# Optimization experiments

Measured on AMD Instinct MI355X. Metric: run time of the kernel, lower is better.

## Reference

```python
import jax, jax.numpy as jnp
import numpy as np

W_ENTROPY, W_MI, W_COV, W_ORTHO, W_L1, W_L2 = 1.0, 0.2, 0.2, 0.1, 0.1, 0.1


def setup_inputs() -> dict:
    key = jax.random.key(0)
    k1, k2, k3, k4 = jax.random.split(key, 4)
    B, NCLS, C = 16384, 1000, 1280
    logits = jax.random.normal(k1, (B, NCLS), dtype=jnp.float32)
    output = jax.nn.log_softmax(logits, axis=1)  # nll_loss expects log-probs
    target = jax.random.randint(k2, (B,), 0, NCLS, dtype=jnp.int64)
    weights = jax.random.normal(k3, (NCLS, C), dtype=jnp.float32) * 0.02
    features = jax.random.normal(k4, (B, C), dtype=jnp.float32)
    return {"output": output, "target": target, "weights": weights, "features": features}


def _kl_loss(features):
    # torch: sum_{i,j} F.kl_div(L[:, i], L[:, j], log_target=True, reduction='mean')
    # kl_div(input, tgt, log_target=True) = mean_b exp(tgt)*(tgt - input)
    # => sum_{i,j,b} P[b,j]*(L[b,j]-L[b,i]) / B
    #  = (C * sum(P*L) - sum(L)) / B   (since sum_j P[b,j] == 1)
    B, C = features.shape
    L = jax.nn.log_softmax(features, axis=1)
    P = jnp.exp(L)
    return (C * jnp.sum(P * L) - jnp.sum(L)) / B


def _cov_loss(features):
    B = features.shape[0]
    cf = features - jnp.mean(features, axis=0, keepdims=True)
    cov = (cf.T @ cf) / B  # [C, C]
    eye = jnp.eye(cov.shape[0], dtype=cov.dtype)
    return jnp.sum((cov - eye) ** 2)  # ||.||_F^2


def _ortho_loss(weights):
    w = weights.reshape(weights.shape[0], -1)
    cov = w @ w.T  # row type
    eye = jnp.eye(cov.shape[0], dtype=cov.dtype)
    return jnp.sum((cov - eye) ** 2)


def reference(output, target, weights, features):
    loss_nll = -jnp.mean(jnp.take_along_axis(output, target[:, None], axis=1))
    loss_kl = _kl_loss(features)
    loss_cov = _cov_loss(features)
    loss_ortho = _ortho_loss(weights)
    loss_l1 = jnp.sum(jnp.abs(weights))
    loss_l2 = jnp.sqrt(jnp.sum(weights ** 2))
    loss = (W_ENTROPY * loss_nll + W_MI * loss_kl + W_COV * loss_cov
            + W_ORTHO * loss_ortho + W_L1 * loss_l1 + W_L2 * loss_l2)
    return loss
```

## Files before the change

### kernel.cpp

```cpp
#include <hip/hip_runtime.h>
#include <stdint.h>
#include <stddef.h>

#define B_N    16384
#define NCLS_N 1000
#define C_N    1280

#define ACC_OFF    0ULL
#define TICKET_OFF 64ULL
#define COLSUM_OFF 128ULL
#define FBT_OFF    8192ULL
#define WB_OFF     41951232ULL
#define G_OFF      44572672ULL
#define H_OFF      51126272ULL

enum { A_NLL = 0, A_KL = 1, A_L1 = 2, A_L2SQ = 3, A_SUMSQF = 4, A_FMU2 = 5, A_GFRO = 6, A_HFRO = 7 };

typedef short s16x8 __attribute__((ext_vector_type(8)));
typedef float f32x4 __attribute__((ext_vector_type(4)));

__device__ __forceinline__ unsigned short f2bf(float f) {
    union { float f; unsigned int u; } v; v.f = f;
    unsigned int u = v.u;
    u += 0x7fffu + ((u >> 16) & 1u);
    return (unsigned short)(u >> 16);
}

__device__ __forceinline__ float wave_red(float v) {
#pragma unroll
    for (int o = 32; o; o >>= 1) v += __shfl_down(v, o, 64);
    return v;
}


__device__ __forceinline__ void nll_body(const float* __restrict__ lp,
                                         const int* __restrict__ tgt,
                                         float* __restrict__ acc, int bidx) {
    int b = bidx * 256 + threadIdx.x;
    int t = tgt[b];
    float v = lp[(size_t)b * NCLS_N + t];
    v = wave_red(v);
    __shared__ float sm_nll[4];
    int wid = threadIdx.x >> 6, lane = threadIdx.x & 63;
    if (lane == 0) sm_nll[wid] = v;
    __syncthreads();
    if (threadIdx.x == 0) atomicAdd(&acc[A_NLL], sm_nll[0] + sm_nll[1] + sm_nll[2] + sm_nll[3]);
}

__device__ __forceinline__ void wpass_body(const float* __restrict__ W,
                                           short* __restrict__ Wb,
                                           float* __restrict__ acc, int idx) {
    int bx = idx & 3;
    int kc = idx >> 2;
    int m = bx * 256 + threadIdx.x;
    bool live = (m < NCLS_N);
    const float4* Wr = (const float4*)(W + (size_t)m * C_N);
    float l1 = 0.f, l2 = 0.f;
#pragma unroll
    for (int kj = 0; kj < 4; kj++) {
        s16x8 pk = { 0, 0, 0, 0, 0, 0, 0, 0 };
        if (live) {
            float4 a = Wr[kc * 8 + kj * 2];
            float4 b = Wr[kc * 8 + kj * 2 + 1];
            l1 += fabsf(a.x) + fabsf(a.y) + fabsf(a.z) + fabsf(a.w)
                + fabsf(b.x) + fabsf(b.y) + fabsf(b.z) + fabsf(b.w);
            l2 += a.x * a.x + a.y * a.y + a.z * a.z + a.w * a.w
                + b.x * b.x + b.y * b.y + b.z * b.z + b.w * b.w;
            pk[0] = (short)f2bf(a.x); pk[1] = (short)f2bf(a.y);
            pk[2] = (short)f2bf(a.z); pk[3] = (short)f2bf(a.w);
            pk[4] = (short)f2bf(b.x); pk[5] = (short)f2bf(b.y);
            pk[6] = (short)f2bf(b.z); pk[7] = (short)f2bf(b.w);
        }
        *(s16x8*)(Wb + ((size_t)(kc * 4 + kj) * 1024 + m) * 8) = pk;
    }
    l1 = wave_red(l1);
    l2 = wave_red(l2);
    __shared__ float sm_w[4][2];
    int wid = threadIdx.x >> 6, lane = threadIdx.x & 63;
    if (lane == 0) { sm_w[wid][0] = l1; sm_w[wid][1] = l2; }
    __syncthreads();
    if (threadIdx.x == 0) {
        atomicAdd(&acc[A_L1],   sm_w[0][0] + sm_w[1][0] + sm_w[2][0] + sm_w[3][0]);
        atomicAdd(&acc[A_L2SQ], sm_w[0][1] + sm_w[1][1] + sm_w[2][1] + sm_w[3][1]);
    }
}

__device__ __forceinline__ void fpass_body(const float* __restrict__ F,
                                           short* __restrict__ Fbt,
                                           float* __restrict__ colsum,
                                           float* __restrict__ acc, int idx) {
    int bx = idx % 5;
    int by = idx / 5;
    int c = bx * 256 + threadIdx.x;
    int kc0 = by * 4;
    float cs = 0.f, sq = 0.f;
    for (int ch = 0; ch < 4; ch++) {
        int kc = kc0 + ch;
        int kbase = kc * 32;
#pragma unroll
        for (int kj = 0; kj < 4; kj++) {
            float v[8];
#pragma unroll
            for (int e = 0; e < 8; e++) v[e] = F[(size_t)(kbase + kj * 8 + e) * C_N + c];
            s16x8 pk;
#pragma unroll
            for (int e = 0; e < 8; e++) {
                cs += v[e];
                sq += v[e] * v[e];
                pk[e] = (short)f2bf(v[e]);
            }
            *(s16x8*)(Fbt + ((size_t)(kc * 4 + kj) * C_N + c) * 8) = pk;
        }
    }
    atomicAdd(&colsum[c], cs);
    sq = wave_red(sq);
    __shared__ float sm_f[4];
    int wid = threadIdx.x >> 6, lane = threadIdx.x & 63;
    if (lane == 0) sm_f[wid] = sq;
    __syncthreads();
    if (threadIdx.x == 0) atomicAdd(&acc[A_SUMSQF], sm_f[0] + sm_f[1] + sm_f[2] + sm_f[3]);
}

__device__ __forceinline__ void klpass_body(const float* __restrict__ F,
                                            float* __restrict__ acc, int idx) {
    int wid = threadIdx.x >> 6, lane = threadIdx.x & 63;
    int gwave = idx * 4 + wid;
    float kl_acc = 0.f;
    for (int b = gwave; b < B_N; b += 4096) {
        const float4* Fr = (const float4*)(F + (size_t)b * C_N);
        float s = 0.f, tt = 0.f, sf = 0.f;
#pragma unroll
        for (int i = 0; i < 5; i++) {
            float4 f = Fr[lane + 64 * i];
            float e0 = __expf(f.x), e1 = __expf(f.y), e2 = __expf(f.z), e3 = __expf(f.w);
            s  += e0 + e1 + e2 + e3;
            tt += e0 * f.x + e1 * f.y + e2 * f.z + e3 * f.w;
            sf += f.x + f.y + f.z + f.w;
        }
        s = wave_red(s); tt = wave_red(tt); sf = wave_red(sf);
        if (lane == 0) kl_acc += (float)C_N * (tt / s) - sf;
    }
    __shared__ float sm_kl[4];
    if (lane == 0) sm_kl[wid] = kl_acc;
    __syncthreads();
    if (threadIdx.x == 0)
        atomicAdd(&acc[A_KL], sm_kl[0] + sm_kl[1] + sm_kl[2] + sm_kl[3]);
}

__device__ __forceinline__ void gram_body(const short* __restrict__ X,
                                          float* __restrict__ S,
                                          int Mp, int T, int tile, int kc_blk, int chunkK) {
    __shared__ __align__(16) short A0[128 * 32];
    __shared__ __align__(16) short A1[128 * 32];
    __shared__ __align__(16) short B0[128 * 32];
    __shared__ __align__(16) short B1[128 * 32];
    int tid = threadIdx.x;
    int bi = 0, rem = tile;
    while (rem >= T - bi) { rem -= T - bi; bi++; }
    int bj = bi + rem;
    int i0 = bi * 128, j0 = bj * 128;

    int wave = tid >> 6, lane = tid & 63;
    int wm = wave >> 1, wn = wave & 1;
    int quad = lane >> 4, l16 = lane & 15;

    const size_t kstep = (size_t)Mp * 32;
    const short *pa0, *pa1, *pb0, *pb1;
    int lo0 = tid * 8, lo1 = (256 + tid) * 8;
    {
        int g0 = tid, g1 = 256 + tid;
        int r0 = g0 >> 2, r1 = g1 >> 2;
        int kj0 = (g0 & 3) ^ (r0 & 3), kj1 = (g1 & 3) ^ (r1 & 3);
        size_t base = (size_t)(kc_blk * chunkK >> 5) * kstep;
        pa0 = X + base + ((size_t)kj0 * Mp + i0 + r0) * 8;
        pa1 = X + base + ((size_t)kj1 * Mp + i0 + r1) * 8;
        pb0 = X + base + ((size_t)kj0 * Mp + j0 + r0) * 8;
        pb1 = X + base + ((size_t)kj1 * Mp + j0 + r1) * 8;
    }

    f32x4 acc[4][4];
#pragma unroll
    for (int i = 0; i < 4; i++)
#pragma unroll
        for (int j = 0; j < 4; j++) acc[i][j] = { 0.f, 0.f, 0.f, 0.f };

    auto stage = [&](short* Ad, short* Bd) {
        __builtin_amdgcn_global_load_lds((const __attribute__((address_space(1))) unsigned int*)pa0,
                                         (__attribute__((address_space(3))) unsigned int*)(Ad + lo0), 16, 0, 0);
        __builtin_amdgcn_global_load_lds((const __attribute__((address_space(1))) unsigned int*)pa1,
                                         (__attribute__((address_space(3))) unsigned int*)(Ad + lo1), 16, 0, 0);
        __builtin_amdgcn_global_load_lds((const __attribute__((address_space(1))) unsigned int*)pb0,
                                         (__attribute__((address_space(3))) unsigned int*)(Bd + lo0), 16, 0, 0);
        __builtin_amdgcn_global_load_lds((const __attribute__((address_space(1))) unsigned int*)pb1,
                                         (__attribute__((address_space(3))) unsigned int*)(Bd + lo1), 16, 0, 0);
        pa0 += kstep; pa1 += kstep; pb0 += kstep; pb1 += kstep;
    };

    auto compute = [&](const short* Ab, const short* Bb) {
        s16x8 af[4], bfr[4];
#pragma unroll
        for (int f = 0; f < 4; f++) {
            int mrow = wm * 64 + f * 16 + l16;
            af[f] = *(const s16x8*)(Ab + mrow * 32 + (quad ^ (mrow & 3)) * 8);
            int nrow = wn * 64 + f * 16 + l16;
            bfr[f] = *(const s16x8*)(Bb + nrow * 32 + (quad ^ (nrow & 3)) * 8);
        }
        __builtin_amdgcn_s_setprio(1);
#pragma unroll
        for (int i = 0; i < 4; i++)
#pragma unroll
            for (int j = 0; j < 4; j++)
                acc[i][j] = __builtin_amdgcn_mfma_f32_16x16x32_bf16(af[i], bfr[j], acc[i][j], 0, 0, 0);
        __builtin_amdgcn_s_setprio(0);
    };

    int nt = chunkK >> 5;
    stage(A0, B0);
    __syncthreads();
    for (int t = 0; t < nt; t += 2) {
        stage(A1, B1);
        compute(A0, B0);
        __syncthreads();
        if (t + 2 < nt) stage(A0, B0);
        compute(A1, B1);
        __syncthreads();
    }

#pragma unroll
    for (int i = 0; i < 4; i++)
#pragma unroll
        for (int j = 0; j < 4; j++)
#pragma unroll
            for (int r = 0; r < 4; r++) {
                int grow = i0 + wm * 64 + i * 16 + quad * 4 + r;
                int gcol = j0 + wn * 64 + j * 16 + l16;
                atomicAdd(&S[(size_t)grow * Mp + gcol], acc[i][j][r]);
            }
}

__device__ __forceinline__ void fro_tile(const float* __restrict__ S,
                                         const float* __restrict__ mu_src,
                                         int Mp, int T, int tile,
                                         float* __restrict__ slotF,
                                         float* __restrict__ slotQ) {
    int bi = 0, rem = tile;
    while (rem >= T - bi) { rem -= T - bi; bi++; }
    int bj = bi + rem;
    size_t base = (size_t)bi * 128 * Mp + (size_t)bj * 128;
    const float invB = 1.f / (float)B_N;
    float sum = 0.f, q = 0.f;
    for (int l = threadIdx.x * 4; l < 128 * 128; l += 1024) {
        int row = l >> 7, col = l & 127;
        float4 v = *(const float4*)(S + base + (size_t)row * Mp + col);
        sum += v.x * v.x + v.y * v.y + v.z * v.z + v.w * v.w;
        if (mu_src) {
            float mr = mu_src[bi * 128 + row] * invB;
            float4 mc = *(const float4*)(mu_src + bj * 128 + col);
            q += mr * (v.x * mc.x + v.y * mc.y + v.z * mc.z + v.w * mc.w) * invB;
        }
    }
    sum = wave_red(sum);
    q = wave_red(q);
    __shared__ float sm_fro[4][2];
    int wid = threadIdx.x >> 6, lane = threadIdx.x & 63;
    if (lane == 0) { sm_fro[wid][0] = sum; sm_fro[wid][1] = q; }
    __syncthreads();
    if (threadIdx.x == 0) {
        float w = (bi == bj) ? 1.f : 2.f;
        atomicAdd(slotF, w * (sm_fro[0][0] + sm_fro[1][0] + sm_fro[2][0] + sm_fro[3][0]));
        if (mu_src)
            atomicAdd(slotQ, w * (sm_fro[0][1] + sm_fro[1][1] + sm_fro[2][1] + sm_fro[3][1]));
    }
}


__global__ __launch_bounds__(256) void prep_kernel(const float* __restrict__ lp,
                                                   const int* __restrict__ tgt,
                                                   const float* __restrict__ W,
                                                   const float* __restrict__ F,
                                                   short* __restrict__ Wb,
                                                   short* __restrict__ Fbt,
                                                   float* __restrict__ colsum,
                                                   float* __restrict__ acc,
                                                   float* __restrict__ G,
                                                   float* __restrict__ H) {
    int b = blockIdx.x;
    if (b < 1024) {
        klpass_body(F, acc, b);
    } else if (b < 1664) {
        fpass_body(F, Fbt, colsum, acc, b - 1024);
    } else if (b < 1824) {
        wpass_body(W, Wb, acc, b - 1664);
    } else if (b < 1888) {
        nll_body(lp, tgt, acc, b - 1824);
    } else if (b < 1988) {
        float4* p = (float4*)G + (size_t)(b - 1888) * 4096;
        float4 z = { 0.f, 0.f, 0.f, 0.f };
        for (int i = threadIdx.x; i < 4096; i += 256) p[i] = z;
    } else {
        float4* p = (float4*)H + (size_t)(b - 1988) * 4096;
        float4 z = { 0.f, 0.f, 0.f, 0.f };
        for (int i = threadIdx.x; i < 4096; i += 256) p[i] = z;
    }
}

__global__ __launch_bounds__(256) void main_kernel(const short* __restrict__ Fbt,
                                                   float* __restrict__ G,
                                                   const short* __restrict__ Wb,
                                                   float* __restrict__ H) {
    int b = blockIdx.x;
    if (b < 880) {
        gram_body(Fbt, G, C_N, 10, b >> 4, b & 15, 1024);
    } else {
        int l = b - 880;
        gram_body(Wb, H, 1024, 8, l >> 2, l & 3, 320);
    }
}

__global__ __launch_bounds__(256) void fro_final_kernel(const float* __restrict__ G,
                                                        const float* __restrict__ H,
                                                        float* __restrict__ acc,
                                                        const float* __restrict__ colsum,
                                                        unsigned* __restrict__ ticket,
                                                        float* __restrict__ out) {
    int b = blockIdx.x;
    if (b < 55) fro_tile(G, colsum, C_N, 10, b, acc + A_GFRO, acc + A_FMU2);
    else        fro_tile(H, nullptr, 1024, 8, b - 55, acc + A_HFRO, nullptr);

    __shared__ int amlast;
    if (threadIdx.x == 0) {
        __threadfence();
        unsigned prev = atomicAdd(ticket, 1u);
        amlast = (prev == 90u);
    }
    __syncthreads();
    if (!amlast) return;
    __threadfence();

    float s = 0.f;
    for (int c = threadIdx.x; c < C_N; c += 256) { float v = colsum[c]; s += v * v; }
    s = wave_red(s);
    __shared__ float sm[4];
    int wid = threadIdx.x >> 6, lane = threadIdx.x & 63;
    if (lane == 0) sm[wid] = s;
    __syncthreads();
    if (threadIdx.x == 0) {
        double musq_raw = (double)(sm[0] + sm[1] + sm[2] + sm[3]);
        double Bd = (double)B_N;
        double gfro = (double)atomicAdd(&acc[A_GFRO], 0.0f);
        double hfro = (double)atomicAdd(&acc[A_HFRO], 0.0f);
        double fmu2 = (double)atomicAdd(&acc[A_FMU2], 0.0f);
        double nll = -((double)acc[A_NLL] / Bd);
        double kl  = (double)acc[A_KL] / Bd;
        double trG = (double)acc[A_SUMSQF];
        double musq = musq_raw / (Bd * Bd);
        double cov = gfro / (Bd * Bd)
                   - (2.0 / Bd) * fmu2
                   + musq * musq
                   - 2.0 * (trG / Bd - musq)
                   + (double)C_N;
        double ortho = hfro - 2.0 * (double)acc[A_L2SQ] + (double)NCLS_N;
        double loss = 1.0 * nll + 0.2 * kl + 0.2 * cov + 0.1 * ortho
                    + 0.1 * (double)acc[A_L1] + 0.1 * sqrt((double)acc[A_L2SQ]);
        out[0] = (float)loss;
    }
}

extern "C" void kernel_launch(void* const* d_in, const int* in_sizes, int n_in,
                              void* d_out, int out_size, void* d_ws, size_t ws_size,
                              hipStream_t stream) {
    (void)in_sizes; (void)n_in; (void)out_size; (void)ws_size;
    const float* output_lp = (const float*)d_in[0];
    const int*   target    = (const int*)d_in[1];
    const float* W         = (const float*)d_in[2];
    const float* F         = (const float*)d_in[3];

    char*     ws     = (char*)d_ws;
    float*    acc    = (float*)(ws + ACC_OFF);
    unsigned* ticket = (unsigned*)(ws + TICKET_OFF);
    float*    colsum = (float*)(ws + COLSUM_OFF);
    short*    Fbt    = (short*)(ws + FBT_OFF);
    short*    Wb     = (short*)(ws + WB_OFF);
    float*    G      = (float*)(ws + G_OFF);
    float*    H      = (float*)(ws + H_OFF);

    hipMemsetAsync(ws, 0, 8192, stream);

    prep_kernel<<<2052, 256, 0, stream>>>(output_lp, target, W, F, Wb, Fbt, colsum, acc, G, H);
    main_kernel<<<1024, 256, 0, stream>>>(Fbt, G, Wb, H);
    fro_final_kernel<<<91, 256, 0, stream>>>(G, H, acc, colsum, ticket, (float*)d_out);
}
```

Measured before the change: 294.9 us.

## Write per-split Gram partials instead of atomics; balance K-split; derive sum(F) from colsum

When the workspace is large enough, each split-K Gram block writes its 128x128 partial tile with plain stores to its own slice, and the Frobenius pass sums the slices. This removes the float atomicAdds and the zeroing of G/H, which prep_kernel no longer needs to do since it launches fewer blocks. In the fallback atomic path, K chunks are unequal to balance triangular tiles. The KL term no longer sums features per row and instead takes sum(F) from colsum in the final kernel. The cost is more workspace, extra partial-slice memory traffic in the final reduction, and a different float summation order.

```diff
diff --git a/kernel.cpp b/kernel.cpp
--- a/kernel.cpp
+++ b/kernel.cpp
@@ -13,6 +13,8 @@
 #define WB_OFF     41951232ULL
 #define G_OFF      44572672ULL
 #define H_OFF      51126272ULL
+#define HP_OFF     102244352ULL
+#define WS_PART_NEED 111681536ULL
 
 enum { A_NLL = 0, A_KL = 1, A_L1 = 2, A_L2SQ = 3, A_SUMSQF = 4, A_FMU2 = 5, A_GFRO = 6, A_HFRO = 7 };
 
@@ -128,17 +130,16 @@
     float kl_acc = 0.f;
     for (int b = gwave; b < B_N; b += 4096) {
         const float4* Fr = (const float4*)(F + (size_t)b * C_N);
-        float s = 0.f, tt = 0.f, sf = 0.f;
+        float s = 0.f, tt = 0.f;
 #pragma unroll
         for (int i = 0; i < 5; i++) {
             float4 f = Fr[lane + 64 * i];
             float e0 = __expf(f.x), e1 = __expf(f.y), e2 = __expf(f.z), e3 = __expf(f.w);
             s  += e0 + e1 + e2 + e3;
             tt += e0 * f.x + e1 * f.y + e2 * f.z + e3 * f.w;
-            sf += f.x + f.y + f.z + f.w;
-        }
-        s = wave_red(s); tt = wave_red(tt); sf = wave_red(sf);
-        if (lane == 0) kl_acc += (float)C_N * (tt / s) - sf;
+        }
+        s = wave_red(s); tt = wave_red(tt);
+        if (lane == 0) kl_acc += (float)C_N * (tt / s);
     }
     __shared__ float sm_kl[4];
     if (lane == 0) sm_kl[wid] = kl_acc;
@@ -147,9 +148,11 @@
         atomicAdd(&acc[A_KL], sm_kl[0] + sm_kl[1] + sm_kl[2] + sm_kl[3]);
 }
 
+template<bool PART>
 __device__ __forceinline__ void gram_body(const short* __restrict__ X,
                                           float* __restrict__ S,
-                                          int Mp, int T, int tile, int kc_blk, int chunkK) {
+                                          int Mp, int T, int ntri,
+                                          int tile, int kc_blk, int k0step, int nt) {
     __shared__ __align__(16) short A0[128 * 32];
     __shared__ __align__(16) short A1[128 * 32];
     __shared__ __align__(16) short B0[128 * 32];
@@ -171,7 +174,7 @@
         int g0 = tid, g1 = 256 + tid;
         int r0 = g0 >> 2, r1 = g1 >> 2;
         int kj0 = (g0 & 3) ^ (r0 & 3), kj1 = (g1 & 3) ^ (r1 & 3);
-        size_t base = (size_t)(kc_blk * chunkK >> 5) * kstep;
+        size_t base = (size_t)k0step * kstep;
         pa0 = X + base + ((size_t)kj0 * Mp + i0 + r0) * 8;
         pa1 = X + base + ((size_t)kj1 * Mp + i0 + r1) * 8;
         pb0 = X + base + ((size_t)kj0 * Mp + j0 + r0) * 8;
@@ -214,7 +217,6 @@
         __builtin_amdgcn_s_setprio(0);
     };
 
-    int nt = chunkK >> 5;
     stage(A0, B0);
     __syncthreads();
     for (int t = 0; t < nt; t += 2) {
@@ -226,32 +228,57 @@
         __syncthreads();
     }
 
-#pragma unroll
-    for (int i = 0; i < 4; i++)
-#pragma unroll
-        for (int j = 0; j < 4; j++)
-#pragma unroll
-            for (int r = 0; r < 4; r++) {
-                int grow = i0 + wm * 64 + i * 16 + quad * 4 + r;
-                int gcol = j0 + wn * 64 + j * 16 + l16;
-                atomicAdd(&S[(size_t)grow * Mp + gcol], acc[i][j][r]);
-            }
-}
-
-__device__ __forceinline__ void fro_tile(const float* __restrict__ S,
-                                         const float* __restrict__ mu_src,
-                                         int Mp, int T, int tile,
-                                         float* __restrict__ slotF,
-                                         float* __restrict__ slotQ) {
+    if (PART) {
+        float* Sp = S + (((size_t)kc_blk * ntri + tile) << 14);
+#pragma unroll
+        for (int i = 0; i < 4; i++)
+#pragma unroll
+            for (int j = 0; j < 4; j++)
+#pragma unroll
+                for (int r = 0; r < 4; r++) {
+                    int lrow = wm * 64 + i * 16 + quad * 4 + r;
+                    int lcol = wn * 64 + j * 16 + l16;
+                    Sp[lrow * 128 + lcol] = acc[i][j][r];
+                }
+    } else {
+#pragma unroll
+        for (int i = 0; i < 4; i++)
+#pragma unroll
+            for (int j = 0; j < 4; j++)
+#pragma unroll
+                for (int r = 0; r < 4; r++) {
+                    int grow = i0 + wm * 64 + i * 16 + quad * 4 + r;
+                    int gcol = j0 + wn * 64 + j * 16 + l16;
+                    atomicAdd(&S[(size_t)grow * Mp + gcol], acc[i][j][r]);
+                }
+    }
+}
+
+__device__ __forceinline__ void fro_tile_any(const float* __restrict__ S,
+                                             const float* __restrict__ mu_src,
+                                             int Mp, int T, int ntri, int tile, int nks, bool part,
+                                             float* __restrict__ slotF,
+                                             float* __restrict__ slotQ) {
     int bi = 0, rem = tile;
     while (rem >= T - bi) { rem -= T - bi; bi++; }
     int bj = bi + rem;
-    size_t base = (size_t)bi * 128 * Mp + (size_t)bj * 128;
+    size_t baseA = (size_t)bi * 128 * Mp + (size_t)bj * 128;
+    const float* baseP = S + ((size_t)tile << 14);
+    size_t pstride = (size_t)ntri << 14;
     const float invB = 1.f / (float)B_N;
     float sum = 0.f, q = 0.f;
     for (int l = threadIdx.x * 4; l < 128 * 128; l += 1024) {
         int row = l >> 7, col = l & 127;
-        float4 v = *(const float4*)(S + base + (size_t)row * Mp + col);
+        float4 v;
+        if (part) {
+            v = *(const float4*)(baseP + l);
+            for (int ks = 1; ks < nks; ks++) {
+                float4 u = *(const float4*)(baseP + (size_t)ks * pstride + l);
+                v.x += u.x; v.y += u.y; v.z += u.z; v.w += u.w;
+            }
+        } else {
+            v = *(const float4*)(S + baseA + (size_t)row * Mp + col);
+        }
         sum += v.x * v.x + v.y * v.y + v.z * v.z + v.w * v.w;
         if (mu_src) {
             float mr = mu_src[bi * 128 + row] * invB;
@@ -304,19 +331,31 @@
     }
 }
 
+template<bool PART>
 __global__ __launch_bounds__(256) void main_kernel(const short* __restrict__ Fbt,
                                                    float* __restrict__ G,
                                                    const short* __restrict__ Wb,
                                                    float* __restrict__ H) {
+    const int G_NT[16] = {18,22,26,30,20,24,28,32,46,42,38,34,44,40,36,32};
+    const int G_K0[16] = {0,18,40,66,96,116,140,168,200,246,288,326,360,404,444,480};
+    const int H_NT[4]  = {8,10,12,10};
+    const int H_K0[4]  = {0,8,18,30};
     int b = blockIdx.x;
     if (b < 880) {
-        gram_body(Fbt, G, C_N, 10, b >> 4, b & 15, 1024);
+        int tile = b >> 4, kc = b & 15;
+        int k0 = PART ? kc * 32 : G_K0[kc];
+        int nt = PART ? 32      : G_NT[kc];
+        gram_body<PART>(Fbt, G, C_N, 10, 55, tile, kc, k0, nt);
     } else {
         int l = b - 880;
-        gram_body(Wb, H, 1024, 8, l >> 2, l & 3, 320);
-    }
-}
-
+        int tile = l >> 2, kc = l & 3;
+        int k0 = PART ? kc * 10 : H_K0[kc];
+        int nt = PART ? 10      : H_NT[kc];
+        gram_body<PART>(Wb, H, 1024, 8, 36, tile, kc, k0, nt);
+    }
+}
+
+template<bool PART>
 __global__ __launch_bounds__(256) void fro_final_kernel(const float* __restrict__ G,
                                                         const float* __restrict__ H,
                                                         float* __restrict__ acc,
@@ -324,8 +363,8 @@
                                                         unsigned* __restrict__ ticket,
                                                         float* __restrict__ out) {
     int b = blockIdx.x;
-    if (b < 55) fro_tile(G, colsum, C_N, 10, b, acc + A_GFRO, acc + A_FMU2);
-    else        fro_tile(H, nullptr, 1024, 8, b - 55, acc + A_HFRO, nullptr);
+    if (b < 55) fro_tile_any(G, colsum, C_N, 10, 55, b, 16, PART, acc + A_GFRO, acc + A_FMU2);
+    else        fro_tile_any(H, nullptr, 1024, 8, 36, b - 55, 4, PART, acc + A_HFRO, nullptr);
 
     __shared__ int amlast;
     if (threadIdx.x == 0) {
@@ -337,21 +376,23 @@
     if (!amlast) return;
     __threadfence();
 
-    float s = 0.f;
-    for (int c = threadIdx.x; c < C_N; c += 256) { float v = colsum[c]; s += v * v; }
+    float s = 0.f, s1 = 0.f;
+    for (int c = threadIdx.x; c < C_N; c += 256) { float v = colsum[c]; s += v * v; s1 += v; }
     s = wave_red(s);
-    __shared__ float sm[4];
-    int wid = threadIdx.x >> 6, lane = threadIdx.x & 63;
-    if (lane == 0) sm[wid] = s;
+    s1 = wave_red(s1);
+    __shared__ float sm[4][2];
+    int wid = threadIdx.x >> 6, lane = threadIdx.x & 63;
+    if (lane == 0) { sm[wid][0] = s; sm[wid][1] = s1; }
     __syncthreads();
     if (threadIdx.x == 0) {
-        double musq_raw = (double)(sm[0] + sm[1] + sm[2] + sm[3]);
+        double musq_raw = (double)(sm[0][0] + sm[1][0] + sm[2][0] + sm[3][0]);
+        double sumF     = (double)(sm[0][1] + sm[1][1] + sm[2][1] + sm[3][1]);
         double Bd = (double)B_N;
         double gfro = (double)atomicAdd(&acc[A_GFRO], 0.0f);
         double hfro = (double)atomicAdd(&acc[A_HFRO], 0.0f);
         double fmu2 = (double)atomicAdd(&acc[A_FMU2], 0.0f);
         double nll = -((double)acc[A_NLL] / Bd);
-        double kl  = (double)acc[A_KL] / Bd;
+        double kl  = ((double)acc[A_KL] - sumF) / Bd;
         double trG = (double)acc[A_SUMSQF];
         double musq = musq_raw / (Bd * Bd);
         double cov = gfro / (Bd * Bd)
@@ -369,7 +410,7 @@
 extern "C" void kernel_launch(void* const* d_in, const int* in_sizes, int n_in,
                               void* d_out, int out_size, void* d_ws, size_t ws_size,
                               hipStream_t stream) {
-    (void)in_sizes; (void)n_in; (void)out_size; (void)ws_size;
+    (void)in_sizes; (void)n_in; (void)out_size;
     const float* output_lp = (const float*)d_in[0];
     const int*   target    = (const int*)d_in[1];
     const float* W         = (const float*)d_in[2];
@@ -381,12 +422,22 @@
     float*    colsum = (float*)(ws + COLSUM_OFF);
     short*    Fbt    = (short*)(ws + FBT_OFF);
     short*    Wb     = (short*)(ws + WB_OFF);
-    float*    G      = (float*)(ws + G_OFF);
-    float*    H      = (float*)(ws + H_OFF);
+
+    bool part = (ws_size >= WS_PART_NEED);
 
     hipMemsetAsync(ws, 0, 8192, stream);
 
-    prep_kernel<<<2052, 256, 0, stream>>>(output_lp, target, W, F, Wb, Fbt, colsum, acc, G, H);
-    main_kernel<<<1024, 256, 0, stream>>>(Fbt, G, Wb, H);
-    fro_final_kernel<<<91, 256, 0, stream>>>(G, H, acc, colsum, ticket, (float*)d_out);
-}
+    if (part) {
+        float* Gp = (float*)(ws + G_OFF);
+        float* Hp = (float*)(ws + HP_OFF);
+        prep_kernel<<<1888, 256, 0, stream>>>(output_lp, target, W, F, Wb, Fbt, colsum, acc, Gp, Hp);
+        main_kernel<true><<<1024, 256, 0, stream>>>(Fbt, Gp, Wb, Hp);
+        fro_final_kernel<true><<<91, 256, 0, stream>>>(Gp, Hp, acc, colsum, ticket, (float*)d_out);
+    } else {
+        float* G = (float*)(ws + G_OFF);
+        float* H = (float*)(ws + H_OFF);
+        prep_kernel<<<2052, 256, 0, stream>>>(output_lp, target, W, F, Wb, Fbt, colsum, acc, G, H);
+        main_kernel<false><<<1024, 256, 0, stream>>>(Fbt, G, Wb, H);
+        fro_final_kernel<false><<<91, 256, 0, stream>>>(G, H, acc, colsum, ticket, (float*)d_out);
+    }
+}
```

Result: faster. 268.5 us (-9.0%).
